# Performance work log

Hardware: AMD Instinct MI355X
Metric: run time of the kernel (lower is better)

Reference implementation:

```python
import jax, jax.numpy as jnp
import numpy as np

N = 500000      # num_edges
D = 128         # embedding_dim
S = 256         # num_samples (negatives)
TEMPERATURE = 0.1
EPS_NORM = 1e-12  # torch F.normalize eps
EPS_COS = 1e-8    # torch F.cosine_similarity eps


def setup_inputs() -> dict:
    key = jax.random.key(0)
    k1, k2, k3 = jax.random.split(key, 3)
    edge_embeddings = jax.random.normal(k1, (N, D), dtype=jnp.float32)
    positive_indices = jax.random.randint(k2, (N,), 0, N, dtype=jnp.int64)
    negative_indices = jax.random.randint(k3, (S,), 0, N, dtype=jnp.int64)
    return {
        "edge_embeddings": edge_embeddings,
        "positive_indices": positive_indices,
        "negative_indices": negative_indices,
    }


def _l2_normalize(x, eps):
    # matches torch: x / max(||x||_2, eps)
    n = jnp.sqrt(jnp.sum(x * x, axis=-1, keepdims=True))
    return x / jnp.maximum(n, eps)


def reference(edge_embeddings, positive_indices, negative_indices):
    # Normalize once; positives reuse the same per-row normalization.
    norm_all = _l2_normalize(edge_embeddings, EPS_NORM)          # [N, D]
    pos_norm = norm_all[positive_indices]                         # [N, D]
    positive_sim = jnp.sum(norm_all * pos_norm, axis=-1)          # [N]

    # cosine_similarity uses eps=1e-8 denominator clamp
    norm_all_cos = _l2_normalize(edge_embeddings, EPS_COS)        # [N, D]
    neg_norm = norm_all_cos[negative_indices]                     # [S, D]
    negative_sim = jnp.einsum('nd,sd->ns', norm_all_cos, neg_norm)  # [N, S]

    positive_logit = positive_sim / TEMPERATURE                   # [N]
    negative_logit = negative_sim / TEMPERATURE                   # [N, S]
    negative = jax.nn.logsumexp(negative_logit, axis=1) - jnp.log(jnp.float32(S))
    loss = -jnp.mean(positive_logit - negative)
    return loss
```

## Files before the change

### kernel.cpp

```cpp
#include <hip/hip_runtime.h>
#include <hip/hip_bf16.h>
#include <math.h>

#define D 128
#define S 256
#define ROWS 64
#define NEG_CHUNK 128
#define LOG_S 5.545177444479562f

typedef __attribute__((ext_vector_type(8)))  short    short8;
typedef __attribute__((ext_vector_type(8)))  __bf16   bf16x8;
typedef __attribute__((ext_vector_type(16))) float    floatx16;

__device__ __forceinline__ unsigned short f2bf(float x) {
  __hip_bfloat16 h = __float2bfloat16(x);
  return *(unsigned short*)&h;
}

__global__ void neg_norm_kernel(const float* __restrict__ emb,
                                const int* __restrict__ negidx,
                                unsigned short* __restrict__ negbf) {
  int s = blockIdx.x;
  int lane = threadIdx.x;
  long idx = (long)negidx[s];
  float2 v = *(const float2*)(emb + idx * D + lane * 2);
  float ss = v.x * v.x + v.y * v.y;
#pragma unroll
  for (int off = 1; off < 64; off <<= 1) ss += __shfl_xor(ss, off);
  float inv = 1.0f / fmaxf(sqrtf(ss), 1e-8f);
  unsigned short o0 = f2bf(v.x * inv), o1 = f2bf(v.y * inv);
  ushort2 o = make_ushort2(o0, o1);
  *(ushort2*)(negbf + s * D + lane * 2) = o;
}

__global__ __launch_bounds__(256, 3)
void hyper_main(const float* __restrict__ emb,
                const int* __restrict__ posidx,
                const unsigned short* __restrict__ negbf,
                double* __restrict__ acc,
                int N) {
  __shared__ __align__(16) char smem[49152];
  unsigned short* rows_l = (unsigned short*)smem;
  unsigned short* negs_l = (unsigned short*)(smem + 16384);

  const int t = threadIdx.x;
  const long rbase = (long)blockIdx.x * ROWS;

  float possum = 0.f;
#pragma unroll
  for (int k = 0; k < 8; ++k) {
    int flat4 = k * 256 + t;
    int r  = flat4 >> 5;
    int c4 = flat4 & 31;
    long n = rbase + r;
    bool valid = (n < (long)N);
    float4 v = make_float4(0.f, 0.f, 0.f, 0.f);
    float4 p = make_float4(0.f, 0.f, 0.f, 0.f);
    if (valid) {
      v = *(const float4*)(emb + n * D + c4 * 4);
      long pi = (long)posidx[n];
      p = *(const float4*)(emb + pi * D + c4 * 4);
    }
    float ssv = v.x*v.x + v.y*v.y + v.z*v.z + v.w*v.w;
    float ssp = p.x*p.x + p.y*p.y + p.z*p.z + p.w*p.w;
    float dp  = v.x*p.x + v.y*p.y + v.z*p.z + v.w*p.w;
#pragma unroll
    for (int off = 1; off < 32; off <<= 1) {
      ssv += __shfl_xor(ssv, off);
      ssp += __shfl_xor(ssp, off);
      dp  += __shfl_xor(dp,  off);
    }
    float inv8 = 1.0f / fmaxf(sqrtf(ssv), 1e-8f);
    ushort4 o = make_ushort4(f2bf(v.x*inv8), f2bf(v.y*inv8),
                             f2bf(v.z*inv8), f2bf(v.w*inv8));
    int u = (c4 >> 1) ^ (r & 15);
    *(ushort4*)&rows_l[r * 128 + u * 8 + (c4 & 1) * 4] = o;
    if ((t & 31) == 0 && valid) {
      float invv = 1.0f / fmaxf(sqrtf(ssv), 1e-12f);
      float invp = 1.0f / fmaxf(sqrtf(ssp), 1e-12f);
      possum += dp * invv * invp * 10.0f;
    }
  }

  const int lane = t & 63;
  const int w  = t >> 6;
  const int q  = lane >> 5;
  const int ln = lane & 31;
  const int tr  = w >> 1;
  const int chh = w & 1;
  const int arow = tr * 32 + ln;
  const int nrow0 = chh * 64 + ln;
  const int nrow1 = chh * 64 + 32 + ln;

  float mrun[16], lrun[16];
#pragma unroll
  for (int i = 0; i < 16; ++i) { mrun[i] = -INFINITY; lrun[i] = 0.f; }

  for (int c = 0; c < 2; ++c) {
    __syncthreads();
#pragma unroll
    for (int k2 = 0; k2 < 8; ++k2) {
      int flat = k2 * 256 + t;
      int nr = flat >> 4;
      int lu = flat & 15;
      uint4 d = *(const uint4*)(negbf + (c * NEG_CHUNK + nr) * D + lu * 8);
      int u = lu ^ (nr & 15);
      *(uint4*)&negs_l[nr * 128 + u * 8] = d;
    }
    __syncthreads();

    floatx16 acc0 = {};
    floatx16 acc1 = {};
#pragma unroll
    for (int ki = 0; ki < 8; ++ki) {
      int lu = ki * 2 + q;
      short8 a  = *(const short8*)&rows_l[arow * 128 + (lu ^ (arow & 15)) * 8];
      short8 b0 = *(const short8*)&negs_l[nrow0 * 128 + (lu ^ (nrow0 & 15)) * 8];
      short8 b1 = *(const short8*)&negs_l[nrow1 * 128 + (lu ^ (nrow1 & 15)) * 8];
      acc0 = __builtin_amdgcn_mfma_f32_32x32x16_bf16(
          __builtin_bit_cast(bf16x8, a), __builtin_bit_cast(bf16x8, b0), acc0, 0, 0, 0);
      acc1 = __builtin_amdgcn_mfma_f32_32x32x16_bf16(
          __builtin_bit_cast(bf16x8, a), __builtin_bit_cast(bf16x8, b1), acc1, 0, 0, 0);
    }

#pragma unroll
    for (int rg = 0; rg < 16; ++rg) {
      float lg0 = acc0[rg] * 10.f;
      float lg1 = acc1[rg] * 10.f;
      float mc = fmaxf(lg0, lg1);
      float mn = fmaxf(mrun[rg], mc);
      lrun[rg] = lrun[rg] * __expf(mrun[rg] - mn)
               + __expf(lg0 - mn) + __expf(lg1 - mn);
      mrun[rg] = mn;
    }
  }

#pragma unroll
  for (int rg = 0; rg < 16; ++rg) {
    float mi = mrun[rg], li = lrun[rg];
#pragma unroll
    for (int off = 1; off < 32; off <<= 1) {
      float mo = __shfl_xor(mi, off);
      float lo = __shfl_xor(li, off);
      float mn = fmaxf(mi, mo);
      li = li * __expf(mi - mn) + lo * __expf(mo - mn);
      mi = mn;
    }
    mrun[rg] = mi; lrun[rg] = li;
  }

  __syncthreads();
  float2* mlbuf = (float2*)smem;
  if (ln == 0) {
#pragma unroll
    for (int rg = 0; rg < 16; ++rg) {
      int r = tr * 32 + (rg & 3) + 8 * (rg >> 2) + 4 * q;
      mlbuf[r * 2 + chh] = make_float2(mrun[rg], lrun[rg]);
    }
  }
  __syncthreads();

  float negterm = 0.f;
  if (t < 64) {
    long n = rbase + t;
    if (n < (long)N) {
      float2 a = mlbuf[t * 2 + 0];
      float2 b = mlbuf[t * 2 + 1];
      float mn = fmaxf(a.x, b.x);
      float l = a.y * __expf(a.x - mn) + b.y * __expf(b.x - mn);
      negterm = mn + __logf(l) - LOG_S;
    }
  }

  float local = negterm - possum;
#pragma unroll
  for (int off = 1; off < 64; off <<= 1) local += __shfl_xor(local, off);
  float* red = (float*)(smem + 2048);
  if (lane == 0) red[w] = local;
  __syncthreads();
  if (t == 0) {
    double tot = (double)red[0] + (double)red[1] +
                 (double)red[2] + (double)red[3];
    atomicAdd(acc, tot);
  }
}

__global__ void finish_kernel(const double* __restrict__ acc,
                              float* __restrict__ out, int N) {
  out[0] = (float)(acc[0] / (double)N);
}

extern "C" void kernel_launch(void* const* d_in, const int* in_sizes, int n_in,
                              void* d_out, int out_size, void* d_ws, size_t ws_size,
                              hipStream_t stream) {
  const float* emb  = (const float*)d_in[0];
  const int* posidx = (const int*)d_in[1];
  const int* negidx = (const int*)d_in[2];
  int N = in_sizes[1];

  double* acc = (double*)d_ws;
  unsigned short* negbf = (unsigned short*)((char*)d_ws + 256);

  hipMemsetAsync(d_ws, 0, 256, stream);
  neg_norm_kernel<<<S, 64, 0, stream>>>(emb, negidx, negbf);
  int grid = (N + ROWS - 1) / ROWS;
  hyper_main<<<grid, 256, 0, stream>>>(emb, posidx, negbf, acc, N);
  finish_kernel<<<1, 1, 0, stream>>>(acc, (float*)d_out, N);
}
```

Baseline: 496.9 us.

## Pre-swizzle negatives, DMA them to LDS, drop online max in logsumexp

The negative-normalize kernel now writes the negatives pre-scaled by 1/T, in bf16, already in the XOR-swizzled LDS layout. The main kernel copies them with global_load_lds (direct global-to-LDS DMA) and issues the second chunk's load during the first chunk's compute. The row loads are reorganised so four threads share one row, which cuts the shuffle reduction from five steps to two and removes the repeated posidx loads. The online max/rescale logsumexp is replaced by a plain sum of exps, since cosine/T is bounded by 10. This relies on that bound and may lose accuracy if the temperature changes.

```diff
diff --git a/kernel.cpp b/kernel.cpp
--- a/kernel.cpp
+++ b/kernel.cpp
@@ -5,13 +5,15 @@
 #define D 128
 #define S 256
 #define ROWS 64
-#define NEG_CHUNK 128
 #define LOG_S 5.545177444479562f
 
 typedef __attribute__((ext_vector_type(8)))  short    short8;
 typedef __attribute__((ext_vector_type(8)))  __bf16   bf16x8;
 typedef __attribute__((ext_vector_type(16))) float    floatx16;
 
+typedef const __attribute__((address_space(1))) void gas_void;
+typedef __attribute__((address_space(3))) void las_void;
+
 __device__ __forceinline__ unsigned short f2bf(float x) {
   __hip_bfloat16 h = __float2bfloat16(x);
   return *(unsigned short*)&h;
@@ -19,24 +21,26 @@
 
 __global__ void neg_norm_kernel(const float* __restrict__ emb,
                                 const int* __restrict__ negidx,
-                                unsigned short* __restrict__ negbf) {
+                                unsigned short* __restrict__ negsw) {
   int s = blockIdx.x;
-  int lane = threadIdx.x;
+  int L = threadIdx.x;
   long idx = (long)negidx[s];
-  float2 v = *(const float2*)(emb + idx * D + lane * 2);
+  float2 v = *(const float2*)(emb + idx * D + L * 2);
   float ss = v.x * v.x + v.y * v.y;
 #pragma unroll
   for (int off = 1; off < 64; off <<= 1) ss += __shfl_xor(ss, off);
-  float inv = 1.0f / fmaxf(sqrtf(ss), 1e-8f);
-  unsigned short o0 = f2bf(v.x * inv), o1 = f2bf(v.y * inv);
-  ushort2 o = make_ushort2(o0, o1);
-  *(ushort2*)(negbf + s * D + lane * 2) = o;
+  float sc = 10.0f / fmaxf(sqrtf(ss), 1e-8f);
+  int chunk = s >> 7, nr = s & 127;
+  int lu = L >> 2, pos = (L & 3) * 2;
+  int u = lu ^ (nr & 15);
+  ushort2 o = make_ushort2(f2bf(v.x * sc), f2bf(v.y * sc));
+  *(ushort2*)(negsw + chunk * 16384 + nr * 128 + u * 8 + pos) = o;
 }
 
 __global__ __launch_bounds__(256, 3)
 void hyper_main(const float* __restrict__ emb,
                 const int* __restrict__ posidx,
-                const unsigned short* __restrict__ negbf,
+                const unsigned short* __restrict__ negsw,
                 double* __restrict__ acc,
                 int N) {
   __shared__ __align__(16) char smem[49152];
@@ -44,77 +48,84 @@
   unsigned short* negs_l = (unsigned short*)(smem + 16384);
 
   const int t = threadIdx.x;
+  const int lane = t & 63;
+  const int w = t >> 6;
   const long rbase = (long)blockIdx.x * ROWS;
 
+  {
+    const char* g = (const char*)negsw + w * 8192 + lane * 16;
+    char* l = (char*)negs_l + w * 8192;
+#pragma unroll
+    for (int i = 0; i < 8; ++i)
+      __builtin_amdgcn_global_load_lds((gas_void*)(g + i * 1024),
+                                       (las_void*)(l + i * 1024), 16, 0, 0);
+  }
+
+  const int r  = t >> 2;
+  const int qq = t & 3;
+  long n = rbase + r;
+  bool valid = (n < (long)N);
+  long pi = 0;
+  if (valid) pi = (long)posidx[n];
+
+  float4 v[8];
+  float ssv = 0.f, ssp = 0.f, dp = 0.f;
+#pragma unroll
+  for (int k = 0; k < 8; ++k) {
+    int c4 = qq + 4 * k;
+    float4 vv = make_float4(0.f, 0.f, 0.f, 0.f);
+    float4 pp = make_float4(0.f, 0.f, 0.f, 0.f);
+    if (valid) {
+      vv = *(const float4*)(emb + n * D + c4 * 4);
+      pp = *(const float4*)(emb + pi * D + c4 * 4);
+    }
+    v[k] = vv;
+    ssv += vv.x*vv.x + vv.y*vv.y + vv.z*vv.z + vv.w*vv.w;
+    ssp += pp.x*pp.x + pp.y*pp.y + pp.z*pp.z + pp.w*pp.w;
+    dp  += vv.x*pp.x + vv.y*pp.y + vv.z*pp.z + vv.w*pp.w;
+  }
+#pragma unroll
+  for (int off = 1; off < 4; off <<= 1) {
+    ssv += __shfl_xor(ssv, off);
+    ssp += __shfl_xor(ssp, off);
+    dp  += __shfl_xor(dp,  off);
+  }
+  float inv8 = 1.0f / fmaxf(sqrtf(ssv), 1e-8f);
+#pragma unroll
+  for (int k = 0; k < 8; ++k) {
+    int c4 = qq + 4 * k;
+    int u = (c4 >> 1) ^ (r & 15);
+    ushort4 o = make_ushort4(f2bf(v[k].x*inv8), f2bf(v[k].y*inv8),
+                             f2bf(v[k].z*inv8), f2bf(v[k].w*inv8));
+    *(ushort4*)&rows_l[r * 128 + u * 8 + (c4 & 1) * 4] = o;
+  }
   float possum = 0.f;
-#pragma unroll
-  for (int k = 0; k < 8; ++k) {
-    int flat4 = k * 256 + t;
-    int r  = flat4 >> 5;
-    int c4 = flat4 & 31;
-    long n = rbase + r;
-    bool valid = (n < (long)N);
-    float4 v = make_float4(0.f, 0.f, 0.f, 0.f);
-    float4 p = make_float4(0.f, 0.f, 0.f, 0.f);
-    if (valid) {
-      v = *(const float4*)(emb + n * D + c4 * 4);
-      long pi = (long)posidx[n];
-      p = *(const float4*)(emb + pi * D + c4 * 4);
-    }
-    float ssv = v.x*v.x + v.y*v.y + v.z*v.z + v.w*v.w;
-    float ssp = p.x*p.x + p.y*p.y + p.z*p.z + p.w*p.w;
-    float dp  = v.x*p.x + v.y*p.y + v.z*p.z + v.w*p.w;
-#pragma unroll
-    for (int off = 1; off < 32; off <<= 1) {
-      ssv += __shfl_xor(ssv, off);
-      ssp += __shfl_xor(ssp, off);
-      dp  += __shfl_xor(dp,  off);
-    }
-    float inv8 = 1.0f / fmaxf(sqrtf(ssv), 1e-8f);
-    ushort4 o = make_ushort4(f2bf(v.x*inv8), f2bf(v.y*inv8),
-                             f2bf(v.z*inv8), f2bf(v.w*inv8));
-    int u = (c4 >> 1) ^ (r & 15);
-    *(ushort4*)&rows_l[r * 128 + u * 8 + (c4 & 1) * 4] = o;
-    if ((t & 31) == 0 && valid) {
-      float invv = 1.0f / fmaxf(sqrtf(ssv), 1e-12f);
-      float invp = 1.0f / fmaxf(sqrtf(ssp), 1e-12f);
-      possum += dp * invv * invp * 10.0f;
-    }
-  }
-
-  const int lane = t & 63;
-  const int w  = t >> 6;
-  const int q  = lane >> 5;
-  const int ln = lane & 31;
+  if (qq == 0 && valid) {
+    float invv = 1.0f / fmaxf(sqrtf(ssv), 1e-12f);
+    float invp = 1.0f / fmaxf(sqrtf(ssp), 1e-12f);
+    possum = dp * invv * invp * 10.0f;
+  }
+
+  const int q   = lane >> 5;
+  const int ln  = lane & 31;
   const int tr  = w >> 1;
   const int chh = w & 1;
-  const int arow = tr * 32 + ln;
+  const int arow  = tr * 32 + ln;
   const int nrow0 = chh * 64 + ln;
-  const int nrow1 = chh * 64 + 32 + ln;
-
-  float mrun[16], lrun[16];
-#pragma unroll
-  for (int i = 0; i < 16; ++i) { mrun[i] = -INFINITY; lrun[i] = 0.f; }
+  const int nrow1 = nrow0 + 32;
+
+  float se[16];
+#pragma unroll
+  for (int i = 0; i < 16; ++i) se[i] = 0.f;
 
   for (int c = 0; c < 2; ++c) {
     __syncthreads();
-#pragma unroll
-    for (int k2 = 0; k2 < 8; ++k2) {
-      int flat = k2 * 256 + t;
-      int nr = flat >> 4;
-      int lu = flat & 15;
-      uint4 d = *(const uint4*)(negbf + (c * NEG_CHUNK + nr) * D + lu * 8);
-      int u = lu ^ (nr & 15);
-      *(uint4*)&negs_l[nr * 128 + u * 8] = d;
-    }
-    __syncthreads();
-
     floatx16 acc0 = {};
     floatx16 acc1 = {};
 #pragma unroll
     for (int ki = 0; ki < 8; ++ki) {
       int lu = ki * 2 + q;
-      short8 a  = *(const short8*)&rows_l[arow * 128 + (lu ^ (arow & 15)) * 8];
+      short8 a  = *(const short8*)&rows_l[arow  * 128 + (lu ^ (arow  & 15)) * 8];
       short8 b0 = *(const short8*)&negs_l[nrow0 * 128 + (lu ^ (nrow0 & 15)) * 8];
       short8 b1 = *(const short8*)&negs_l[nrow1 * 128 + (lu ^ (nrow1 & 15)) * 8];
       acc0 = __builtin_amdgcn_mfma_f32_32x32x16_bf16(
@@ -122,54 +133,44 @@
       acc1 = __builtin_amdgcn_mfma_f32_32x32x16_bf16(
           __builtin_bit_cast(bf16x8, a), __builtin_bit_cast(bf16x8, b1), acc1, 0, 0, 0);
     }
-
+    if (c == 0) {
+      __syncthreads();
+      const char* g = (const char*)negsw + 32768 + w * 8192 + lane * 16;
+      char* l = (char*)negs_l + w * 8192;
+#pragma unroll
+      for (int i = 0; i < 8; ++i)
+        __builtin_amdgcn_global_load_lds((gas_void*)(g + i * 1024),
+                                         (las_void*)(l + i * 1024), 16, 0, 0);
+    }
+#pragma unroll
+    for (int rg = 0; rg < 16; ++rg)
+      se[rg] += __expf(acc0[rg]) + __expf(acc1[rg]);
+  }
+
+#pragma unroll
+  for (int rg = 0; rg < 16; ++rg) {
+    float sv = se[rg];
+#pragma unroll
+    for (int off = 1; off < 32; off <<= 1) sv += __shfl_xor(sv, off);
+    se[rg] = sv;
+  }
+
+  __syncthreads();
+  float* sebuf = (float*)smem;
+  if (ln == 0) {
 #pragma unroll
     for (int rg = 0; rg < 16; ++rg) {
-      float lg0 = acc0[rg] * 10.f;
-      float lg1 = acc1[rg] * 10.f;
-      float mc = fmaxf(lg0, lg1);
-      float mn = fmaxf(mrun[rg], mc);
-      lrun[rg] = lrun[rg] * __expf(mrun[rg] - mn)
-               + __expf(lg0 - mn) + __expf(lg1 - mn);
-      mrun[rg] = mn;
-    }
-  }
-
-#pragma unroll
-  for (int rg = 0; rg < 16; ++rg) {
-    float mi = mrun[rg], li = lrun[rg];
-#pragma unroll
-    for (int off = 1; off < 32; off <<= 1) {
-      float mo = __shfl_xor(mi, off);
-      float lo = __shfl_xor(li, off);
-      float mn = fmaxf(mi, mo);
-      li = li * __expf(mi - mn) + lo * __expf(mo - mn);
-      mi = mn;
-    }
-    mrun[rg] = mi; lrun[rg] = li;
-  }
-
-  __syncthreads();
-  float2* mlbuf = (float2*)smem;
-  if (ln == 0) {
-#pragma unroll
-    for (int rg = 0; rg < 16; ++rg) {
-      int r = tr * 32 + (rg & 3) + 8 * (rg >> 2) + 4 * q;
-      mlbuf[r * 2 + chh] = make_float2(mrun[rg], lrun[rg]);
+      int rr = tr * 32 + (rg & 3) + 8 * (rg >> 2) + 4 * q;
+      sebuf[rr * 2 + chh] = se[rg];
     }
   }
   __syncthreads();
 
   float negterm = 0.f;
   if (t < 64) {
-    long n = rbase + t;
-    if (n < (long)N) {
-      float2 a = mlbuf[t * 2 + 0];
-      float2 b = mlbuf[t * 2 + 1];
-      float mn = fmaxf(a.x, b.x);
-      float l = a.y * __expf(a.x - mn) + b.y * __expf(b.x - mn);
-      negterm = mn + __logf(l) - LOG_S;
-    }
+    long n2 = rbase + t;
+    if (n2 < (long)N)
+      negterm = __logf(sebuf[t * 2] + sebuf[t * 2 + 1]) - LOG_S;
   }
 
   float local = negterm - possum;
@@ -199,11 +200,11 @@
   int N = in_sizes[1];
 
   double* acc = (double*)d_ws;
-  unsigned short* negbf = (unsigned short*)((char*)d_ws + 256);
+  unsigned short* negsw = (unsigned short*)((char*)d_ws + 256);
 
   hipMemsetAsync(d_ws, 0, 256, stream);
-  neg_norm_kernel<<<S, 64, 0, stream>>>(emb, negidx, negbf);
+  neg_norm_kernel<<<S, 64, 0, stream>>>(emb, negidx, negsw);
   int grid = (N + ROWS - 1) / ROWS;
-  hyper_main<<<grid, 256, 0, stream>>>(emb, posidx, negbf, acc, N);
+  hyper_main<<<grid, 256, 0, stream>>>(emb, posidx, negsw, acc, N);
   finish_kernel<<<1, 1, 0, stream>>>(acc, (float*)d_out, N);
 }
```

After: 411.8 us. 17.1% less time.
